# Kernel tuning notes

Hardware: AMD Instinct MI355X
Metric: run time of the kernel (lower is better)

## Reference

```python
import jax, jax.numpy as jnp
import numpy as np

SPIKE_THRESH = 0.95  # matches docstring example: torch.rand(...) > 0.95 sparse spikes


def setup_inputs() -> dict:
    key = jax.random.key(0)
    k1, k2 = jax.random.split(key)
    H, BATCH, N, B, T = 8, 4, 4096, 4, 512
    z0 = jnp.zeros((H, BATCH, N, B), dtype=jnp.float32)
    # sparse binary spikes over T timesteps
    spikes = (jax.random.uniform(k1, (T, BATCH, N)) > SPIKE_THRESH).astype(jnp.float32)
    taus = jnp.array([2.0, 4.0, 8.0, 16.0], dtype=jnp.float32)
    coeffs = jax.random.normal(k2, (H, B), dtype=jnp.float32)
    return {"z0": z0, "spikes": spikes, "taus": taus, "coeffs": coeffs, "dt": 1}


def reference(z0, spikes, taus, coeffs, dt):
    # z0:     [H, batch, N, B]   initial basis states (TemporalBasis.init_state)
    # spikes: [T, batch, N]      input spikes per timestep
    # taus:   [B]                basis time constants (ms)
    # coeffs: [H, B]             per-head mixing coefficients
    decay = jnp.exp(-jnp.float32(dt) / taus)  # [B], time-invariant

    def step(z, s_t):
        # TemporalBasis.step: decay * z + broadcast(spikes)
        z_new = decay * z + s_t[None, :, :, None]  # [H, batch, N, B]
        # TemporalBasis.get_response: weighted sum over basis kernels
        resp = jnp.einsum('hbnk,hk->hbn', z_new, coeffs)  # [H, batch, N]
        return z_new, resp

    _, responses = jax.lax.scan(step, z0, spikes)
    return responses  # [T, H, batch, N]
```

## Files before the change

### kernel.cpp

```cpp
#include <hip/hip_runtime.h>

#define HH 8
#define BB 4
#define TT 512
#define CHUNKS 16
#define LL (TT / CHUNKS)
#define SPB 64

__global__ __launch_bounds__(CHUNKS * SPB)
void temporal_basis_kernel(const float* __restrict__ z0,
                           const float* __restrict__ spikes,
                           const float* __restrict__ taus,
                           const float* __restrict__ coeffs,
                           const int* __restrict__ dt_p,
                           float* __restrict__ out,
                           int S) {
    __shared__ float4 lds_P[CHUNKS][SPB];

    const int chunk = threadIdx.x >> 6;
    const int sl    = threadIdx.x & 63;
    const int site  = blockIdx.x * SPB + sl;

    const float dt = (float)dt_p[0];
    float d[BB];
#pragma unroll
    for (int k = 0; k < BB; ++k) d[k] = expf(-dt / taus[k]);

    const int t0 = chunk * LL;
    float P[BB] = {0.f, 0.f, 0.f, 0.f};
    unsigned mask = 0u;
    const float* __restrict__ sp = spikes + (size_t)t0 * S + site;
#pragma unroll
    for (int i = 0; i < LL; ++i) {
        const float s = sp[(size_t)i * S];
        mask |= (s != 0.f ? 1u : 0u) << i;
#pragma unroll
        for (int k = 0; k < BB; ++k) P[k] = d[k] * P[k] + s;
    }
    lds_P[chunk][sl] = make_float4(P[0], P[1], P[2], P[3]);
    __syncthreads();

    float dL[BB];
#pragma unroll
    for (int k = 0; k < BB; ++k) {
        float x = d[k];
        x = x * x; x = x * x; x = x * x; x = x * x; x = x * x;
        dL[k] = x;
    }

    float A[BB] = {0.f, 0.f, 0.f, 0.f};
    for (int e = 0; e < chunk; ++e) {
        const float4 p = lds_P[e][sl];
        A[0] = dL[0] * A[0] + p.x;
        A[1] = dL[1] * A[1] + p.y;
        A[2] = dL[2] * A[2] + p.z;
        A[3] = dL[3] * A[3] + p.w;
    }

    float dt0[BB] = {1.f, 1.f, 1.f, 1.f};
    for (int e = 0; e < chunk; ++e) {
#pragma unroll
        for (int k = 0; k < BB; ++k) dt0[k] *= dL[k];
    }

    float z[HH][BB];
#pragma unroll
    for (int h = 0; h < HH; ++h) {
        const float4 zv = ((const float4*)z0)[(size_t)h * S + site];
        z[h][0] = dt0[0] * zv.x + A[0];
        z[h][1] = dt0[1] * zv.y + A[1];
        z[h][2] = dt0[2] * zv.z + A[2];
        z[h][3] = dt0[3] * zv.w + A[3];
    }

    float c[HH][BB];
#pragma unroll
    for (int h = 0; h < HH; ++h)
#pragma unroll
        for (int k = 0; k < BB; ++k) c[h][k] = coeffs[h * BB + k];

    float* __restrict__ op = out + (size_t)t0 * HH * S + site;
#pragma unroll 4
    for (int i = 0; i < LL; ++i) {
        const float s = (mask & (1u << i)) ? 1.0f : 0.0f;
#pragma unroll
        for (int h = 0; h < HH; ++h) {
#pragma unroll
            for (int k = 0; k < BB; ++k) z[h][k] = d[k] * z[h][k] + s;
            const float r = z[h][0] * c[h][0] + z[h][1] * c[h][1] +
                            z[h][2] * c[h][2] + z[h][3] * c[h][3];
            __builtin_nontemporal_store(r, &op[(size_t)(i * HH + h) * S]);
        }
    }
}

extern "C" void kernel_launch(void* const* d_in, const int* in_sizes, int n_in,
                              void* d_out, int out_size, void* d_ws, size_t ws_size,
                              hipStream_t stream) {
    const float* z0     = (const float*)d_in[0];
    const float* spikes = (const float*)d_in[1];
    const float* taus   = (const float*)d_in[2];
    const float* coeffs = (const float*)d_in[3];
    const int*   dt_p   = (const int*)d_in[4];
    float* out = (float*)d_out;

    const int S = in_sizes[1] / TT;
    const int grid = S / SPB;

    temporal_basis_kernel<<<grid, CHUNKS * SPB, 0, stream>>>(
        z0, spikes, taus, coeffs, dt_p, out, S);
}
```

Baseline: 301.0 us.

## Split chunked scan into separate prefix and replay kernels via workspace

Splits the single fused kernel into two launches. The first computes per-chunk spike masks and prefix carry states and writes them to a workspace buffer. The second replays each (chunk, site-block) as its own 1024-thread block and emits the outputs. This removes the shared-memory sync coupling between the store-heavy output phase and the scan phase, and gives the replay more blocks and different output access locality. In exchange it adds a second launch and a global-memory round trip for the intermediates. It falls back to the fused kernel when the workspace is too small.

```diff
diff --git a/kernel.cpp b/kernel.cpp
--- a/kernel.cpp
+++ b/kernel.cpp
@@ -6,6 +6,126 @@
 #define CHUNKS 16
 #define LL (TT / CHUNKS)
 #define SPB 64
+#define K2T 1024
+
+__global__ __launch_bounds__(CHUNKS * SPB)
+void tb_scan(const float* __restrict__ spikes,
+             const float* __restrict__ taus,
+             const int* __restrict__ dt_p,
+             float4* __restrict__ Abuf,
+             unsigned int* __restrict__ Mbuf,
+             int S) {
+    __shared__ float4 lds_P[CHUNKS][SPB];
+
+    const int chunk = threadIdx.x >> 6;
+    const int sl    = threadIdx.x & 63;
+    const int site  = blockIdx.x * SPB + sl;
+
+    const float dt = (float)dt_p[0];
+    float d[BB];
+#pragma unroll
+    for (int k = 0; k < BB; ++k) d[k] = expf(-dt / taus[k]);
+
+    const int t0 = chunk * LL;
+    float P[BB] = {0.f, 0.f, 0.f, 0.f};
+    unsigned mask = 0u;
+    const float* __restrict__ sp = spikes + (size_t)t0 * S + site;
+#pragma unroll
+    for (int i = 0; i < LL; ++i) {
+        const float s = sp[(size_t)i * S];
+        mask |= (s != 0.f ? 1u : 0u) << i;
+#pragma unroll
+        for (int k = 0; k < BB; ++k) P[k] = d[k] * P[k] + s;
+    }
+    Mbuf[(size_t)chunk * S + site] = mask;
+    lds_P[chunk][sl] = make_float4(P[0], P[1], P[2], P[3]);
+    __syncthreads();
+
+    float dL[BB];
+#pragma unroll
+    for (int k = 0; k < BB; ++k) {
+        float x = d[k];
+        x = x * x; x = x * x; x = x * x; x = x * x; x = x * x;
+        dL[k] = x;
+    }
+
+    float A[BB] = {0.f, 0.f, 0.f, 0.f};
+    for (int e = 0; e < chunk; ++e) {
+        const float4 p = lds_P[e][sl];
+        A[0] = dL[0] * A[0] + p.x;
+        A[1] = dL[1] * A[1] + p.y;
+        A[2] = dL[2] * A[2] + p.z;
+        A[3] = dL[3] * A[3] + p.w;
+    }
+    Abuf[(size_t)chunk * S + site] = make_float4(A[0], A[1], A[2], A[3]);
+}
+
+__global__ __launch_bounds__(K2T)
+void tb_replay(const float* __restrict__ z0,
+               const float* __restrict__ taus,
+               const float* __restrict__ coeffs,
+               const int* __restrict__ dt_p,
+               const float4* __restrict__ Abuf,
+               const unsigned int* __restrict__ Mbuf,
+               float* __restrict__ out,
+               int S) {
+    const int nsb   = S / K2T;
+    const int chunk = blockIdx.x / nsb;
+    const int sb    = blockIdx.x - chunk * nsb;
+    const int site  = sb * K2T + threadIdx.x;
+    const int t0    = chunk * LL;
+
+    const float dt = (float)dt_p[0];
+    float d[BB];
+#pragma unroll
+    for (int k = 0; k < BB; ++k) d[k] = expf(-dt / taus[k]);
+
+    float dL[BB];
+#pragma unroll
+    for (int k = 0; k < BB; ++k) {
+        float x = d[k];
+        x = x * x; x = x * x; x = x * x; x = x * x; x = x * x;
+        dL[k] = x;
+    }
+    float dt0[BB] = {1.f, 1.f, 1.f, 1.f};
+    for (int e = 0; e < chunk; ++e) {
+#pragma unroll
+        for (int k = 0; k < BB; ++k) dt0[k] *= dL[k];
+    }
+
+    const float4 Av = Abuf[(size_t)chunk * S + site];
+    unsigned mask = Mbuf[(size_t)chunk * S + site];
+
+    float z[HH][BB];
+#pragma unroll
+    for (int h = 0; h < HH; ++h) {
+        const float4 zv = ((const float4*)z0)[(size_t)h * S + site];
+        z[h][0] = dt0[0] * zv.x + Av.x;
+        z[h][1] = dt0[1] * zv.y + Av.y;
+        z[h][2] = dt0[2] * zv.z + Av.z;
+        z[h][3] = dt0[3] * zv.w + Av.w;
+    }
+
+    float c[HH][BB];
+#pragma unroll
+    for (int h = 0; h < HH; ++h)
+#pragma unroll
+        for (int k = 0; k < BB; ++k) c[h][k] = coeffs[h * BB + k];
+
+    float* __restrict__ op = out + (size_t)t0 * HH * S + site;
+#pragma unroll 4
+    for (int i = 0; i < LL; ++i) {
+        const float s = (mask & (1u << i)) ? 1.0f : 0.0f;
+#pragma unroll
+        for (int h = 0; h < HH; ++h) {
+#pragma unroll
+            for (int k = 0; k < BB; ++k) z[h][k] = d[k] * z[h][k] + s;
+            const float r = z[h][0] * c[h][0] + z[h][1] * c[h][1] +
+                            z[h][2] * c[h][2] + z[h][3] * c[h][3];
+            __builtin_nontemporal_store(r, &op[(size_t)(i * HH + h) * S]);
+        }
+    }
+}
 
 __global__ __launch_bounds__(CHUNKS * SPB)
 void temporal_basis_kernel(const float* __restrict__ z0,
@@ -105,8 +225,22 @@
     float* out = (float*)d_out;
 
     const int S = in_sizes[1] / TT;
-    const int grid = S / SPB;
-
-    temporal_basis_kernel<<<grid, CHUNKS * SPB, 0, stream>>>(
-        z0, spikes, taus, coeffs, dt_p, out, S);
-}
+
+    const size_t abytes = (size_t)CHUNKS * S * sizeof(float4);
+    const size_t mbytes = (size_t)CHUNKS * S * sizeof(unsigned);
+
+    if (d_ws != nullptr && ws_size >= abytes + mbytes) {
+        float4* Abuf       = (float4*)d_ws;
+        unsigned int* Mbuf = (unsigned int*)((char*)d_ws + abytes);
+
+        tb_scan<<<S / SPB, CHUNKS * SPB, 0, stream>>>(
+            spikes, taus, dt_p, Abuf, Mbuf, S);
+
+        const int grid2 = CHUNKS * (S / K2T);
+        tb_replay<<<grid2, K2T, 0, stream>>>(
+            z0, taus, coeffs, dt_p, Abuf, Mbuf, out, S);
+    } else {
+        temporal_basis_kernel<<<S / SPB, CHUNKS * SPB, 0, stream>>>(
+            z0, spikes, taus, coeffs, dt_p, out, S);
+    }
+}
```

After: 333.8 us. +10.9%, slower.
